# Kernel optimization log

Hardware: AMD Instinct MI355X
Metric: run time of the kernel (lower is better)

## Reference

```python
import jax, jax.numpy as jnp
import numpy as np

B, C, N, D = 4, 128, 4096, 128  # batch, channels (=d_tran=out), points
BN_EPS = 1e-5


def setup_inputs() -> dict:
    key = jax.random.key(0)
    ks = jax.random.split(key, 10)
    s = 1.0 / np.sqrt(C)
    return {
        "x": jax.random.normal(ks[0], (B, C, N), dtype=jnp.float32),
        "Wqk": jax.random.uniform(ks[1], (D, C), minval=-s, maxval=s, dtype=jnp.float32),  # shared q/k weight
        "Wv": jax.random.uniform(ks[2], (D, C), minval=-s, maxval=s, dtype=jnp.float32),
        "bv": jax.random.uniform(ks[3], (D,), minval=-s, maxval=s, dtype=jnp.float32),
        "Wt": jax.random.uniform(ks[4], (C, D), minval=-s, maxval=s, dtype=jnp.float32),
        "bt": jax.random.uniform(ks[5], (C,), minval=-s, maxval=s, dtype=jnp.float32),
        "gamma": jnp.ones((C,), dtype=jnp.float32) + 0.1 * jax.random.normal(ks[6], (C,), dtype=jnp.float32),
        "beta": 0.1 * jax.random.normal(ks[7], (C,), dtype=jnp.float32),
        "rmean": 0.1 * jax.random.normal(ks[8], (C,), dtype=jnp.float32),
        "rvar": jax.random.uniform(ks[9], (C,), minval=0.5, maxval=1.5, dtype=jnp.float32),
    }


def reference(x, Wqk, Wv, bv, Wt, bt, gamma, beta, rmean, rvar):
    # x: [B, C, N]; 1x1 convs are per-point matmuls over the channel dim.
    x_q = jnp.einsum('dc,bcn->bnd', Wqk, x)                 # [B, N, D]
    x_k = jnp.einsum('dc,bcn->bdn', Wqk, x)                 # [B, D, N] (tied weight)
    x_v = jnp.einsum('dc,bcn->bdn', Wv, x) + bv[None, :, None]
    energy = jnp.einsum('bnd,bdm->bnm', x_q, x_k)           # [B, N, N]
    attention = jax.nn.softmax(energy, axis=-1)             # row softmax
    attention = attention / (1e-9 + attention.sum(axis=1, keepdims=True))  # L1 over columns
    x_r = jnp.einsum('bdn,bnm->bdm', x_v, attention)        # [B, D, N]
    y = jnp.einsum('od,bdn->bon', Wt, x - x_r) + bt[None, :, None]
    # BatchNorm1d, inference mode (running stats)
    y = gamma[None, :, None] * (y - rmean[None, :, None]) * jax.lax.rsqrt(rvar[None, :, None] + BN_EPS) + beta[None, :, None]
    return x + jax.nn.relu(y)
```

## Files before the change

kernel.cpp:

```cpp
#include <hip/hip_runtime.h>
#include <hip/hip_bf16.h>

typedef unsigned int u32;
typedef unsigned short u16;
using bf16x8 = __attribute__((ext_vector_type(8))) short;
using f32x4  = __attribute__((ext_vector_type(4))) float;
using f32x16 = __attribute__((ext_vector_type(16))) float;

#define B_ 4
#define C_ 128
#define N_ 4096
#define D_ 128
#define NS 8
#define NSEG (N_ / NS)

#define QS_STRIDE 136
#define VS_STRIDE 40

__device__ __forceinline__ u16 f2bf(float f) {
    u32 x = __builtin_bit_cast(u32, f);
    x = x + 0x7fffu + ((x >> 16) & 1u);
    return (u16)(x >> 16);
}
__device__ __forceinline__ float bf2f(u16 h) {
    return __builtin_bit_cast(float, (u32)h << 16);
}
__device__ __forceinline__ u32 cvtpk(float lo, float hi) {
    u32 d;
    asm("v_cvt_pk_bf16_f32 %0, %1, %2" : "=v"(d) : "v"(lo), "v"(hi));
    return d;
}
#define EXP2 __builtin_amdgcn_exp2f
__device__ __forceinline__ bf16x8 pack8(const float* v, float s) {
    bf16x8 r;
#pragma unroll
    for (int j = 0; j < 8; ++j) r[j] = (short)f2bf(v[j] * s);
    return r;
}

__global__ __launch_bounds__(256) void k_proj(
        const float* __restrict__ x, const float* __restrict__ Wqk,
        const float* __restrict__ Wv, const float* __restrict__ bv,
        u16* __restrict__ Qbf, u16* __restrict__ Vbf) {
    __shared__ float xs[C_ * 65];
    const int bid = blockIdx.x;
    const int b  = bid >> 6;
    const int n0 = (bid & 63) << 6;
    const int t  = threadIdx.x;
    const float* xb = x + (size_t)b * C_ * N_;
    for (int i = 0; i < 32; ++i) {
        int idx = i * 256 + t;
        int c = idx >> 6, n = idx & 63;
        xs[c * 65 + n] = xb[(size_t)c * N_ + n0 + n];
    }
    __syncthreads();
    const int lane = t & 63, w = t >> 6;
    const int l15 = lane & 15, g = lane >> 4;
    const float SC = 1.2011224087864498f;

    bf16x8 xf[4];
#pragma unroll
    for (int kk = 0; kk < 4; ++kk) {
        float tmp[8];
#pragma unroll
        for (int j = 0; j < 8; ++j) tmp[j] = xs[(kk * 32 + g * 8 + j) * 65 + (16 * w + l15)];
        xf[kk] = pack8(tmp, 1.0f);
    }
    for (int dt = 0; dt < 8; ++dt) {
        const int d = dt * 16 + l15;
        bf16x8 wq[4], wv[4];
#pragma unroll
        for (int kk = 0; kk < 4; ++kk) {
            const float* pq = Wqk + (size_t)d * C_ + kk * 32 + g * 8;
            const float* pv = Wv  + (size_t)d * C_ + kk * 32 + g * 8;
            float a[8], c8[8];
#pragma unroll
            for (int j = 0; j < 8; ++j) { a[j] = pq[j]; c8[j] = pv[j]; }
            wq[kk] = pack8(a, SC);
            wv[kk] = pack8(c8, 1.0f);
        }
        f32x4 aq = {0.f, 0.f, 0.f, 0.f}, av = {0.f, 0.f, 0.f, 0.f};
#pragma unroll
        for (int kk = 0; kk < 4; ++kk) {
            aq = __builtin_amdgcn_mfma_f32_16x16x32_bf16(xf[kk], wq[kk], aq, 0, 0, 0);
            av = __builtin_amdgcn_mfma_f32_16x16x32_bf16(wv[kk], xf[kk], av, 0, 0, 0);
        }
#pragma unroll
        for (int r = 0; r < 4; ++r) {
            int nn = n0 + 16 * w + g * 4 + r;
            Qbf[((size_t)b * N_ + nn) * D_ + dt * 16 + l15] = f2bf(aq[r]);
            int dd = dt * 16 + g * 4 + r;
            Vbf[((size_t)b * D_ + dd) * N_ + n0 + 16 * w + l15] = f2bf(av[r] + bv[dd]);
        }
    }
}

__global__ __launch_bounds__(256, 4) void k_pass1(const u16* __restrict__ Qbf,
                                                  float* __restrict__ rsp) {
    __shared__ __align__(16) u16 qs[2][32 * QS_STRIDE];
    int bid = blockIdx.x;
    const int s = bid & 7; bid >>= 3;
    const int ntile = bid & 31; const int b = bid >> 5;
    const int t = threadIdx.x, lane = t & 63, w = t >> 6;
    const int l31 = lane & 31, hi = lane >> 5;
    const int nb = ntile * 128 + w * 32;

    bf16x8 bqn[8];
    {
        const u16* qn = Qbf + ((size_t)b * N_ + nb + l31) * D_ + hi * 8;
#pragma unroll
        for (int dblk = 0; dblk < 8; ++dblk) bqn[dblk] = *(const bf16x8*)(qn + dblk * 16);
    }
    const int srow = t >> 4, sslot = t & 15;
    const u16* qsrc = Qbf + ((size_t)b * N_ + s * NSEG + srow) * D_ + sslot * 8;
    const int qoff = srow * QS_STRIDE + sslot * 8;

    {
        uint4 a0 = *(const uint4*)qsrc;
        uint4 a1 = *(const uint4*)(qsrc + (size_t)16 * D_);
        *(uint4*)&qs[0][qoff] = a0;
        *(uint4*)&qs[0][qoff + 16 * QS_STRIDE] = a1;
    }
    __syncthreads();

    float rs0 = 0.f, rs1 = 0.f;
    for (int mc = 0; mc < NSEG / 32; ++mc) {
        const int cur = mc & 1;
        uint4 qpre0, qpre1;
        if (mc < NSEG / 32 - 1) {
            qpre0 = *(const uint4*)(qsrc + (size_t)(mc + 1) * 32 * D_);
            qpre1 = *(const uint4*)(qsrc + (size_t)((mc + 1) * 32 + 16) * D_);
        }
        f32x16 ea, eb;
#pragma unroll
        for (int i = 0; i < 16; ++i) { ea[i] = 0.f; eb[i] = 0.f; }
#pragma unroll
        for (int dblk = 0; dblk < 4; ++dblk) {
            bf16x8 am0 = *(const bf16x8*)(qs[cur] + l31 * QS_STRIDE + (2 * dblk + hi) * 8);
            bf16x8 am1 = *(const bf16x8*)(qs[cur] + l31 * QS_STRIDE + (2 * (dblk + 4) + hi) * 8);
            ea = __builtin_amdgcn_mfma_f32_32x32x16_bf16(am0, bqn[dblk], ea, 0, 0, 0);
            eb = __builtin_amdgcn_mfma_f32_32x32x16_bf16(am1, bqn[dblk + 4], eb, 0, 0, 0);
        }
#pragma unroll
        for (int r = 0; r < 16; r += 2) {
            rs0 += EXP2(ea[r] + eb[r] - 64.0f);
            rs1 += EXP2(ea[r + 1] + eb[r + 1] - 64.0f);
        }
        if (mc < NSEG / 32 - 1) {
            *(uint4*)&qs[cur ^ 1][qoff] = qpre0;
            *(uint4*)&qs[cur ^ 1][qoff + 16 * QS_STRIDE] = qpre1;
        }
        __syncthreads();
    }
    float rs = rs0 + rs1;
    rs += __shfl_xor(rs, 32);
    if (lane < 32) rsp[((size_t)s * B_ + b) * N_ + nb + l31] = rs;
}

__global__ void k_irs(const float* __restrict__ rsp, float* __restrict__ irs) {
    int i = blockIdx.x * 256 + threadIdx.x;
    if (i < B_ * N_) {
        float s = 0.f;
#pragma unroll
        for (int sp = 0; sp < NS; ++sp) s += rsp[(size_t)sp * B_ * N_ + i];
        irs[i] = 1.0f / s;
    }
}

__global__ __launch_bounds__(256, 3) void k_pass2(
        const u16* __restrict__ Qbf, const u16* __restrict__ Vbf,
        const float* __restrict__ irs, u32* __restrict__ Rp32,
        float* __restrict__ csp) {
    __shared__ __align__(16) u16 qs[2][32 * QS_STRIDE];
    __shared__ __align__(16) u16 vs[2][128 * VS_STRIDE];
    int bid = blockIdx.x;
    const int s = bid & 7; bid >>= 3;
    const int mtile = bid & 31; const int b = bid >> 5;
    const int t = threadIdx.x, lane = t & 63, w = t >> 6;
    const int l31 = lane & 31, hi = lane >> 5;
    const int m0 = mtile * 128 + w * 32;

    bf16x8 bq[8];
    {
        const u16* qm = Qbf + ((size_t)b * N_ + m0 + l31) * D_ + hi * 8;
#pragma unroll
        for (int dblk = 0; dblk < 8; ++dblk) bq[dblk] = *(const bf16x8*)(qm + dblk * 16);
    }
    f32x16 acc[4];
#pragma unroll
    for (int i = 0; i < 4; ++i)
#pragma unroll
        for (int r = 0; r < 16; ++r) acc[i][r] = 0.f;
    float cs = 0.f;
    const float* irsb = irs + (size_t)b * N_;

    const int qrow = t >> 4, qslot = t & 15;
    const u16* qsrc = Qbf + ((size_t)b * N_ + s * NSEG + qrow) * D_ + qslot * 8;
    const int qoff = qrow * QS_STRIDE + qslot * 8;
    const int vd = t >> 2, vslot = t & 3;
    const u16* vsrc = Vbf + ((size_t)b * D_ + vd) * N_ + s * NSEG + vslot * 8;
    const int voff = vd * VS_STRIDE + vslot * 8;

    {
        uint4 a0 = *(const uint4*)qsrc;
        uint4 a1 = *(const uint4*)(qsrc + (size_t)16 * D_);
        uint4 b0 = *(const uint4*)vsrc;
        uint4 b1 = *(const uint4*)(vsrc + (size_t)64 * N_);
        *(uint4*)&qs[0][qoff] = a0;
        *(uint4*)&qs[0][qoff + 16 * QS_STRIDE] = a1;
        *(uint4*)&vs[0][voff] = b0;
        *(uint4*)&vs[0][voff + 64 * VS_STRIDE] = b1;
    }
    __syncthreads();

    for (int nc = 0; nc < NSEG / 32; ++nc) {
        const int cur = nc & 1;
        const int nb = s * NSEG + nc * 32;
        uint4 qpre0, qpre1, vpre0, vpre1;
        if (nc < NSEG / 32 - 1) {
            qpre0 = *(const uint4*)(qsrc + (size_t)(nc + 1) * 32 * D_);
            qpre1 = *(const uint4*)(qsrc + (size_t)((nc + 1) * 32 + 16) * D_);
            vpre0 = *(const uint4*)(vsrc + (nc + 1) * 32);
            vpre1 = *(const uint4*)(vsrc + (size_t)64 * N_ + (nc + 1) * 32);
        }
        const float* irp = irsb + nb;
        float si[32];
#pragma unroll
        for (int j = 0; j < 32; ++j) si[j] = irp[j];

        f32x16 ea, eb;
#pragma unroll
        for (int i = 0; i < 16; ++i) { ea[i] = 0.f; eb[i] = 0.f; }
#pragma unroll
        for (int dblk = 0; dblk < 4; ++dblk) {
            bf16x8 aq0 = *(const bf16x8*)(qs[cur] + l31 * QS_STRIDE + (2 * dblk + hi) * 8);
            bf16x8 aq1 = *(const bf16x8*)(qs[cur] + l31 * QS_STRIDE + (2 * (dblk + 4) + hi) * 8);
            ea = __builtin_amdgcn_mfma_f32_32x32x16_bf16(aq0, bq[dblk], ea, 0, 0, 0);
            eb = __builtin_amdgcn_mfma_f32_32x32x16_bf16(aq1, bq[dblk + 4], eb, 0, 0, 0);
        }
        uint4 bpA0, bpA1;
        {
            u32 A[8];
#pragma unroll
            for (int i = 0; i < 8; ++i) {
                const int c = 2 * (i & 1) + 8 * (i >> 1);
                float ir0 = hi ? si[c + 4] : si[c];
                float ir1 = hi ? si[c + 5] : si[c + 1];
                float p0 = EXP2(ea[2 * i] + eb[2 * i] - 64.0f) * ir0;
                float p1 = EXP2(ea[2 * i + 1] + eb[2 * i + 1] - 64.0f) * ir1;
                cs += p0 + p1;
                A[i] = cvtpk(p0, p1);
            }
            u32 X0 = (u32)__shfl_xor((int)A[0], 32), X1 = (u32)__shfl_xor((int)A[1], 32);
            u32 X2 = (u32)__shfl_xor((int)A[2], 32), X3 = (u32)__shfl_xor((int)A[3], 32);
            u32 X4 = (u32)__shfl_xor((int)A[4], 32), X5 = (u32)__shfl_xor((int)A[5], 32);
            u32 X6 = (u32)__shfl_xor((int)A[6], 32), X7 = (u32)__shfl_xor((int)A[7], 32);
            bpA0 = (uint4){hi ? X2 : A[0], hi ? X3 : A[1], hi ? A[2] : X0, hi ? A[3] : X1};
            bpA1 = (uint4){hi ? X6 : A[4], hi ? X7 : A[5], hi ? A[6] : X4, hi ? A[7] : X5};
        }
#pragma unroll
        for (int nblk = 0; nblk < 2; ++nblk) {
            bf16x8 bp = __builtin_bit_cast(bf16x8, nblk ? bpA1 : bpA0);
#pragma unroll
            for (int dblk = 0; dblk < 4; ++dblk) {
                bf16x8 av = *(const bf16x8*)(vs[cur] + (dblk * 32 + l31) * VS_STRIDE +
                                             (nblk * 2 + hi) * 8);
                acc[dblk] = __builtin_amdgcn_mfma_f32_32x32x16_bf16(av, bp, acc[dblk], 0, 0, 0);
            }
        }
        if (nc < NSEG / 32 - 1) {
            *(uint4*)&qs[cur ^ 1][qoff] = qpre0;
            *(uint4*)&qs[cur ^ 1][qoff + 16 * QS_STRIDE] = qpre1;
            *(uint4*)&vs[cur ^ 1][voff] = vpre0;
            *(uint4*)&vs[cur ^ 1][voff + 64 * VS_STRIDE] = vpre1;
        }
        __syncthreads();
    }
    cs += __shfl_xor(cs, 32);
    if (lane < 32) csp[((size_t)s * B_ + b) * N_ + m0 + l31] = cs;
    u32* rpb = Rp32 + ((size_t)s * B_ + b) * (size_t)(D_ / 2) * N_;
#pragma unroll
    for (int dblk = 0; dblk < 4; ++dblk) {
#pragma unroll
        for (int j = 0; j < 8; ++j) {
            const int row = dblk * 16 + (j & 1) + 4 * (j >> 1) + 2 * hi;
            u32 pk = cvtpk(acc[dblk][2 * j], acc[dblk][2 * j + 1]);
            rpb[(size_t)row * N_ + m0 + l31] = pk;
        }
    }
}

__global__ __launch_bounds__(512) void k_final(
        const float* __restrict__ x, const float* __restrict__ Wt,
        const float* __restrict__ bt, const float* __restrict__ gamma,
        const float* __restrict__ beta, const float* __restrict__ rmean,
        const float* __restrict__ rvar, const u32* __restrict__ Rp32,
        const float* __restrict__ csp, float* __restrict__ out) {
    __shared__ float us[128 * 65];
    __shared__ float icss[64];
    const int bid = blockIdx.x;
    const int b = bid >> 6;
    const int n0 = (bid & 63) << 6;
    const int t = threadIdx.x, lane = t & 63, w = t >> 6;
    const int l15 = lane & 15, g = lane >> 4;
    if (t < 64) {
        float s = 0.f;
#pragma unroll
        for (int sp = 0; sp < NS; ++sp)
            s += csp[((size_t)sp * B_ + b) * N_ + n0 + t];
        icss[t] = 1.0f / (1e-9f + s);
    }
    __syncthreads();
    const float* xb = x + (size_t)b * C_ * N_;
    for (int i = 0; i < 8; ++i) {
        int idx = i * 512 + t;
        int dp = idx >> 6, n = idx & 63;
        float r0 = 0.f, r1 = 0.f;
#pragma unroll
        for (int sp = 0; sp < NS; ++sp) {
            u32 v = Rp32[(((size_t)(sp * B_ + b) * (D_ / 2)) + dp) * N_ + n0 + n];
            r0 += bf2f((u16)(v & 0xffffu));
            r1 += bf2f((u16)(v >> 16));
        }
        float ic = icss[n];
        us[(2 * dp) * 65 + n]     = xb[(size_t)(2 * dp) * N_ + n0 + n]     - r0 * ic;
        us[(2 * dp + 1) * 65 + n] = xb[(size_t)(2 * dp + 1) * N_ + n0 + n] - r1 * ic;
    }
    __syncthreads();
    const int cg = w & 3;
    const int ct0 = (w >> 2) * 4;
    bf16x8 uf[4];
#pragma unroll
    for (int kk = 0; kk < 4; ++kk) {
        float tmp[8];
#pragma unroll
        for (int j = 0; j < 8; ++j) tmp[j] = us[(kk * 32 + g * 8 + j) * 65 + (16 * cg + l15)];
        uf[kk] = pack8(tmp, 1.0f);
    }
    for (int cti = 0; cti < 4; ++cti) {
        const int ct = ct0 + cti;
        const int c = ct * 16 + l15;
        bf16x8 wf[4];
#pragma unroll
        for (int kk = 0; kk < 4; ++kk) {
            const float* p = Wt + (size_t)c * D_ + kk * 32 + g * 8;
            float a[8];
#pragma unroll
            for (int j = 0; j < 8; ++j) a[j] = p[j];
            wf[kk] = pack8(a, 1.0f);
        }
        f32x4 acc = {0.f, 0.f, 0.f, 0.f};
#pragma unroll
        for (int kk = 0; kk < 4; ++kk)
            acc = __builtin_amdgcn_mfma_f32_16x16x32_bf16(wf[kk], uf[kk], acc, 0, 0, 0);
#pragma unroll
        for (int r = 0; r < 4; ++r) {
            const int cc = ct * 16 + g * 4 + r;
            const int nn = n0 + 16 * cg + l15;
            float y = acc[r] + bt[cc];
            float bn = gamma[cc] * (y - rmean[cc]) * rsqrtf(rvar[cc] + 1e-5f) + beta[cc];
            float rl = fmaxf(bn, 0.0f);
            out[((size_t)b * C_ + cc) * N_ + nn] = xb[(size_t)cc * N_ + nn] + rl;
        }
    }
}

extern "C" void kernel_launch(void* const* d_in, const int* in_sizes, int n_in,
                              void* d_out, int out_size, void* d_ws, size_t ws_size,
                              hipStream_t stream) {
    (void)in_sizes; (void)n_in; (void)out_size; (void)ws_size;
    const float* x     = (const float*)d_in[0];
    const float* Wqk   = (const float*)d_in[1];
    const float* Wv    = (const float*)d_in[2];
    const float* bv    = (const float*)d_in[3];
    const float* Wt    = (const float*)d_in[4];
    const float* bt    = (const float*)d_in[5];
    const float* gamma = (const float*)d_in[6];
    const float* beta  = (const float*)d_in[7];
    const float* rmean = (const float*)d_in[8];
    const float* rvar  = (const float*)d_in[9];
    float* out = (float*)d_out;

    char* ws = (char*)d_ws;
    u16*   Qbf = (u16*)(ws);
    u16*   Vbf = (u16*)(ws + 4194304);
    float* rsp = (float*)(ws + 8388608);
    float* irs = (float*)(ws + 8912896);
    float* csp = (float*)(ws + 8978432);
    u32*   Rp  = (u32*)(ws + 9502720);

    k_proj  <<<B_ * 64,      256, 0, stream>>>(x, Wqk, Wv, bv, Qbf, Vbf);
    k_pass1 <<<B_ * 32 * NS, 256, 0, stream>>>(Qbf, rsp);
    k_irs   <<<(B_ * N_ + 255) / 256, 256, 0, stream>>>(rsp, irs);
    k_pass2 <<<B_ * 32 * NS, 256, 0, stream>>>(Qbf, Vbf, irs, Rp, csp);
    k_final <<<B_ * 64,      512, 0, stream>>>(x, Wt, bt, gamma, beta, rmean, rvar, Rp, csp, out);
}
```

Before: 119.7 us.

## Software-pipeline PV MFMA one chunk behind QK and softmax in pass2

Restructures the pass2 loop so the P·V MFMAs for the previous chunk are issued while the current chunk's QK MFMAs and exp/softmax work proceed, using a triple-buffered V tile in LDS and carrying the packed P fragments across iterations. A drain step after the loop handles the last chunk. The goal is to overlap the dependent exp/shuffle latency with matrix-core work. In exchange it uses more LDS and keeps more registers live, which could reduce occupancy at launch_bounds(256,3).

New measurement: 118.9 us (median of 2 runs). Within noise of the previous version (-0.7%).

```diff
diff --git a/kernel.cpp b/kernel.cpp
--- a/kernel.cpp
+++ b/kernel.cpp
@@ -13,6 +13,7 @@
 #define D_ 128
 #define NS 8
 #define NSEG (N_ / NS)
+#define NCH (NSEG / 32)
 
 #define QS_STRIDE 136
 #define VS_STRIDE 40
@@ -124,10 +125,10 @@
     __syncthreads();
 
     float rs0 = 0.f, rs1 = 0.f;
-    for (int mc = 0; mc < NSEG / 32; ++mc) {
+    for (int mc = 0; mc < NCH; ++mc) {
         const int cur = mc & 1;
         uint4 qpre0, qpre1;
-        if (mc < NSEG / 32 - 1) {
+        if (mc < NCH - 1) {
             qpre0 = *(const uint4*)(qsrc + (size_t)(mc + 1) * 32 * D_);
             qpre1 = *(const uint4*)(qsrc + (size_t)((mc + 1) * 32 + 16) * D_);
         }
@@ -146,7 +147,7 @@
             rs0 += EXP2(ea[r] + eb[r] - 64.0f);
             rs1 += EXP2(ea[r + 1] + eb[r + 1] - 64.0f);
         }
-        if (mc < NSEG / 32 - 1) {
+        if (mc < NCH - 1) {
             *(uint4*)&qs[cur ^ 1][qoff] = qpre0;
             *(uint4*)&qs[cur ^ 1][qoff + 16 * QS_STRIDE] = qpre1;
         }
@@ -172,7 +173,7 @@
         const float* __restrict__ irs, u32* __restrict__ Rp32,
         float* __restrict__ csp) {
     __shared__ __align__(16) u16 qs[2][32 * QS_STRIDE];
-    __shared__ __align__(16) u16 vs[2][128 * VS_STRIDE];
+    __shared__ __align__(16) u16 vs[3][128 * VS_STRIDE];
     int bid = blockIdx.x;
     const int s = bid & 7; bid >>= 3;
     const int mtile = bid & 31; const int b = bid >> 5;
@@ -213,11 +214,14 @@
     }
     __syncthreads();
 
-    for (int nc = 0; nc < NSEG / 32; ++nc) {
+    uint4 bpP0, bpP1;
+    int vm1 = 2, vp1 = 1;
+
+    for (int nc = 0; nc < NCH; ++nc) {
         const int cur = nc & 1;
         const int nb = s * NSEG + nc * 32;
         uint4 qpre0, qpre1, vpre0, vpre1;
-        if (nc < NSEG / 32 - 1) {
+        if (nc < NCH - 1) {
             qpre0 = *(const uint4*)(qsrc + (size_t)(nc + 1) * 32 * D_);
             qpre1 = *(const uint4*)(qsrc + (size_t)((nc + 1) * 32 + 16) * D_);
             vpre0 = *(const uint4*)(vsrc + (nc + 1) * 32);
@@ -238,7 +242,18 @@
             ea = __builtin_amdgcn_mfma_f32_32x32x16_bf16(aq0, bq[dblk], ea, 0, 0, 0);
             eb = __builtin_amdgcn_mfma_f32_32x32x16_bf16(aq1, bq[dblk + 4], eb, 0, 0, 0);
         }
-        uint4 bpA0, bpA1;
+        if (nc > 0) {
+#pragma unroll
+            for (int nblk = 0; nblk < 2; ++nblk) {
+                bf16x8 bp = __builtin_bit_cast(bf16x8, nblk ? bpP1 : bpP0);
+#pragma unroll
+                for (int dblk = 0; dblk < 4; ++dblk) {
+                    bf16x8 av = *(const bf16x8*)(vs[vm1] + (dblk * 32 + l31) * VS_STRIDE +
+                                                 (nblk * 2 + hi) * 8);
+                    acc[dblk] = __builtin_amdgcn_mfma_f32_32x32x16_bf16(av, bp, acc[dblk], 0, 0, 0);
+                }
+            }
+        }
         {
             u32 A[8];
 #pragma unroll
@@ -255,26 +270,30 @@
             u32 X2 = (u32)__shfl_xor((int)A[2], 32), X3 = (u32)__shfl_xor((int)A[3], 32);
             u32 X4 = (u32)__shfl_xor((int)A[4], 32), X5 = (u32)__shfl_xor((int)A[5], 32);
             u32 X6 = (u32)__shfl_xor((int)A[6], 32), X7 = (u32)__shfl_xor((int)A[7], 32);
-            bpA0 = (uint4){hi ? X2 : A[0], hi ? X3 : A[1], hi ? A[2] : X0, hi ? A[3] : X1};
-            bpA1 = (uint4){hi ? X6 : A[4], hi ? X7 : A[5], hi ? A[6] : X4, hi ? A[7] : X5};
-        }
+            bpP0 = (uint4){hi ? X2 : A[0], hi ? X3 : A[1], hi ? A[2] : X0, hi ? A[3] : X1};
+            bpP1 = (uint4){hi ? X6 : A[4], hi ? X7 : A[5], hi ? A[6] : X4, hi ? A[7] : X5};
+        }
+        if (nc < NCH - 1) {
+            *(uint4*)&qs[cur ^ 1][qoff] = qpre0;
+            *(uint4*)&qs[cur ^ 1][qoff + 16 * QS_STRIDE] = qpre1;
+            *(uint4*)&vs[vp1][voff] = vpre0;
+            *(uint4*)&vs[vp1][voff + 64 * VS_STRIDE] = vpre1;
+        }
+        __syncthreads();
+        vm1 = (vm1 == 2) ? 0 : vm1 + 1;
+        vp1 = (vp1 == 2) ? 0 : vp1 + 1;
+    }
+    {
 #pragma unroll
         for (int nblk = 0; nblk < 2; ++nblk) {
-            bf16x8 bp = __builtin_bit_cast(bf16x8, nblk ? bpA1 : bpA0);
+            bf16x8 bp = __builtin_bit_cast(bf16x8, nblk ? bpP1 : bpP0);
 #pragma unroll
             for (int dblk = 0; dblk < 4; ++dblk) {
-                bf16x8 av = *(const bf16x8*)(vs[cur] + (dblk * 32 + l31) * VS_STRIDE +
+                bf16x8 av = *(const bf16x8*)(vs[vm1] + (dblk * 32 + l31) * VS_STRIDE +
                                              (nblk * 2 + hi) * 8);
                 acc[dblk] = __builtin_amdgcn_mfma_f32_32x32x16_bf16(av, bp, acc[dblk], 0, 0, 0);
             }
         }
-        if (nc < NSEG / 32 - 1) {
-            *(uint4*)&qs[cur ^ 1][qoff] = qpre0;
-            *(uint4*)&qs[cur ^ 1][qoff + 16 * QS_STRIDE] = qpre1;
-            *(uint4*)&vs[cur ^ 1][voff] = vpre0;
-            *(uint4*)&vs[cur ^ 1][voff + 64 * VS_STRIDE] = vpre1;
-        }
-        __syncthreads();
     }
     cs += __shfl_xor(cs, 32);
     if (lane < 32) csp[((size_t)s * B_ + b) * N_ + m0 + l31] = cs;
```
